# Performance work log

Hardware: AMD Instinct MI355X
Metric: run time of the kernel (lower is better)

The kernel has to match this reference:

```python
import jax, jax.numpy as jnp
import numpy as np

N = 32768   # nodes
E = 131072  # directed edges
B = 8       # graphs in batch
F_IN = 1025
NEG = -1e30
EPS = 1e-5


def _lin_init(k, i, o):
    k1, k2 = jax.random.split(k)
    s = 1.0 / np.sqrt(i)
    return (jax.random.uniform(k1, (i, o), jnp.float32, -s, s),
            jax.random.uniform(k2, (o,), jnp.float32, -s, s))


def _bn_init(k, c):
    k1, k2, k3, k4 = jax.random.split(k, 4)
    gamma = jax.random.uniform(k1, (c,), jnp.float32, 0.5, 1.5)
    beta = jax.random.normal(k2, (c,), jnp.float32) * 0.1
    mean = jax.random.normal(k3, (c,), jnp.float32) * 0.1
    var = jax.random.uniform(k4, (c,), jnp.float32, 0.5, 1.5)
    return jnp.stack([gamma, beta, mean, var])  # [4, c]


def setup_inputs() -> dict:
    key = jax.random.key(0)
    ks = jax.random.split(key, 16)
    x = jax.random.normal(ks[0], (N, F_IN), jnp.float32)
    edge_index = jax.random.randint(ks[1], (2, E), 0, N, dtype=jnp.int32)
    batch = jnp.sort(jax.random.randint(ks[2], (N,), 0, B, dtype=jnp.int32))
    pool_w, pool_b = _lin_init(ks[3], 2 * F_IN, 1)
    c1_w0, _ = _lin_init(ks[4], F_IN, 512)
    c1_w1, c1_b = _lin_init(ks[5], F_IN, 512)
    c2_w0, _ = _lin_init(ks[6], 512, 512)
    c2_w1, c2_b = _lin_init(ks[7], 512, 512)
    bn1 = _bn_init(ks[8], 512)
    bn2 = _bn_init(ks[9], 512)
    bn3 = _bn_init(ks[10], 512)
    bn4 = _bn_init(ks[11], 256)
    lin1_w, lin1_b = _lin_init(ks[12], 1024, 512)
    lin2_w, lin2_b = _lin_init(ks[13], 512, 256)
    lin3_w, lin3_b = _lin_init(ks[14], 256, 4)
    return dict(x=x, edge_index=edge_index, batch=batch,
                pool_w=pool_w, pool_b=pool_b,
                c1_w0=c1_w0, c1_w1=c1_w1, c1_b=c1_b,
                c2_w0=c2_w0, c2_w1=c2_w1, c2_b=c2_b,
                bn1=bn1, bn2=bn2, bn3=bn3, bn4=bn4,
                lin1_w=lin1_w, lin1_b=lin1_b,
                lin2_w=lin2_w, lin2_b=lin2_b,
                lin3_w=lin3_w, lin3_b=lin3_b)


def _batchnorm(h, p):
    g, b, m, v = p[0], p[1], p[2], p[3]
    return (h - m) * jax.lax.rsqrt(v + EPS) * g + b


def _cheb(h, row, col, w, w0, w1, b):
    # ChebConv K=2, sym norm, lambda_max=2: out = h@W0 + (L_hat h)@W1 + b,
    # L_hat = -D^{-1/2} A D^{-1/2} (self-loops removed, diag of scaled L is 0)
    deg = jax.ops.segment_sum(w, row, num_segments=N)
    dis = jnp.where(deg > 0, 1.0 / jnp.sqrt(jnp.maximum(deg, 1e-12)), 0.0)
    nrm = -w * dis[row] * dis[col]
    tx1 = jax.ops.segment_sum(nrm[:, None] * h[row], col, num_segments=N)
    return h @ w0 + tx1 @ w1 + b


def _forward(x, edge_index, batch, pool_w, pool_b,
             c1_w0, c1_w1, c1_b, c2_w0, c2_w1, c2_b,
             bn1, bn2, bn3, bn4,
             lin1_w, lin1_b, lin2_w, lin2_b, lin3_w, lin3_b):
    u, v = edge_index[0], edge_index[1]

    # ---- EdgePooling: edge scores = softmax over dst segments, +0.5 ----
    e = (jnp.concatenate([x[u], x[v]], axis=1) @ pool_w + pool_b)[:, 0]  # [E]
    m = jax.ops.segment_max(e, v, num_segments=N)
    ex = jnp.exp(e - m[v])
    score = ex / jax.ops.segment_sum(ex, v, num_segments=N)[v] + 0.5

    # ---- greedy maximal matching in descending score order ----
    order = jnp.argsort(-score)

    def step(used, k):
        uu, vv = u[k], v[k]
        ok = jnp.logical_not(used[uu] | used[vv])
        used = used.at[uu].set(used[uu] | ok)
        used = used.at[vv].set(used[vv] | ok)
        return used, ok

    _, ok_sorted = jax.lax.scan(step, jnp.zeros((N,), bool), order)
    sel = jnp.zeros((E,), bool).at[order].set(ok_sorted)

    rep = jnp.minimum(u, v)  # cluster representative of a merged edge
    cluster = jnp.arange(N, dtype=jnp.int32)
    cluster = cluster.at[jnp.where(sel, u, N)].set(rep, mode='drop')
    cluster = cluster.at[jnp.where(sel, v, N)].set(rep, mode='drop')
    node_score = jnp.ones((N,), x.dtype).at[jnp.where(sel, rep, N)].set(score, mode='drop')
    px = jnp.zeros_like(x).at[cluster].add(x) * node_score[:, None]  # pooled node feats
    valid = cluster == jnp.arange(N, dtype=jnp.int32)  # surviving cluster rows

    # ---- coarsened edge_index, coalesced (dedup), self-loops dropped ----
    cu, cv = cluster[u], cluster[v]
    nonloop = cu != cv
    key = jnp.where(nonloop, cu * N + cv, N * N + jnp.arange(E, dtype=jnp.int32))
    o2 = jnp.argsort(key)
    sk = key[o2]
    first = jnp.concatenate([jnp.ones((1,), bool), sk[1:] != sk[:-1]])
    keep_sorted = first & (sk < N * N)
    w = jnp.zeros((E,), x.dtype).at[o2].set(keep_sorted.astype(x.dtype))

    # ---- two ChebConv + BN(eval) + ReLU ----
    h = jax.nn.relu(_batchnorm(_cheb(px, cu, cv, w, c1_w0, c1_w1, c1_b), bn1))
    h = jax.nn.relu(_batchnorm(_cheb(h, cu, cv, w, c2_w0, c2_w1, c2_b), bn2))

    # ---- global max + mean pool over valid nodes per graph ----
    hmax = jax.ops.segment_max(jnp.where(valid[:, None], h, NEG), batch, num_segments=B)
    cnt = jax.ops.segment_sum(valid.astype(h.dtype), batch, num_segments=B)
    hmean = jax.ops.segment_sum(jnp.where(valid[:, None], h, 0.0), batch,
                                num_segments=B) / jnp.maximum(cnt, 1.0)[:, None]
    g = jnp.concatenate([hmax, hmean], axis=1)  # [B, 1024]

    # ---- readout MLP (dropout off in eval) ----
    g = jax.nn.relu(_batchnorm(g @ lin1_w + lin1_b, bn3))
    g = jax.nn.relu(_batchnorm(g @ lin2_w + lin2_b, bn4))
    feature = g
    out = jax.nn.log_softmax(jax.nn.relu(g @ lin3_w + lin3_b), axis=-1)
    return out, feature


def reference(x, edge_index, batch, pool_w, pool_b,
              c1_w0, c1_w1, c1_b, c2_w0, c2_w1, c2_b,
              bn1, bn2, bn3, bn4,
              lin1_w, lin1_b, lin2_w, lin2_b, lin3_w, lin3_b):
    return _forward(x, edge_index, batch, pool_w, pool_b,
                    c1_w0, c1_w1, c1_b, c2_w0, c2_w1, c2_b,
                    bn1, bn2, bn3, bn4,
                    lin1_w, lin1_b, lin2_w, lin2_b, lin3_w, lin3_b)
```

## Files before the change

kernel.cpp:

```cpp
#include <hip/hip_runtime.h>
#include <hip/hip_bf16.h>
#include <cstdint>
#include <cmath>

typedef unsigned int u32;
typedef unsigned long long u64;
typedef float f32x4 __attribute__((ext_vector_type(4)));
typedef __bf16 bf16x8 __attribute__((ext_vector_type(8)));
typedef unsigned short us8 __attribute__((ext_vector_type(8)));
typedef unsigned short us4 __attribute__((ext_vector_type(4)));

#define NN 32768
#define NE 131072
#define FIN 1025
#define HTS 262144
#define HTM (HTS - 1)

#define WS_A_D    0ul
#define WS_B_D    262144ul
#define WS_EMAX   524288ul
#define WS_SSUM   655360ul
#define WS_EXD    917504ul
#define WS_CIN    917504ul
#define WS_KEY    1966080ul
#define WS_BEST   3014656ul
#define WS_USED   3276800ul
#define WS_CUR    3276800ul
#define WS_ACT0   3407872ul
#define WS_ACT1   3932160ul
#define WS_BTHI   0ul
#define WS_BT2    3407872ul
#define WS_HT     1966080ul
#define WS_RACC1  2097152ul
#define WS_RACC2  2113536ul
#define WS_CIDX   2129920ul
#define WS_PERM   2260992ul
#define WS_SCORE  4456448ul
#define WS_CSRA   4456448ul
#define WS_SEL    4980736ul
#define WS_CSRC   4980736ul
#define WS_CLUST  5505024ul
#define WS_OTHER  5636096ul
#define WS_NSC    5767168ul
#define WS_CEU    5898240ul
#define WS_CEV    6422528ul
#define WS_DEG    6946816ul
#define WS_OFF    6946816ul
#define WS_DIS    7077888ul
#define WS_PXL    7077888ul
#define WS_MISC   7208960ul
#define WS_GMAX   7209216ul
#define WS_GSUM   7225600ul
#define WS_GCNT   7241984ul
#define WS_P      7242240ul
#define WS_PB     74351104ul
#define WS_H      141459968ul

__device__ __forceinline__ u32 enc_f(float f) {
    u32 b = __float_as_uint(f);
    return (b & 0x80000000u) ? ~b : (b | 0x80000000u);
}
__device__ __forceinline__ float dec_f(u32 m) {
    return (m & 0x80000000u) ? __uint_as_float(m ^ 0x80000000u) : __uint_as_float(~m);
}
__device__ __forceinline__ double wave_sum(double v) {
    #pragma unroll
    for (int off = 32; off > 0; off >>= 1) v += __shfl_down(v, off, 64);
    return v;
}
__device__ __forceinline__ unsigned short f2bf(float v) {
    u32 b = __float_as_uint(v);
    u32 r = b + 0x7FFFu + ((b >> 16) & 1u);
    return (unsigned short)(r >> 16);
}
__device__ __forceinline__ float bf2f(unsigned short h) {
    return __uint_as_float(((u32)h) << 16);
}
__device__ __forceinline__ bf16x8 ld_frag(const unsigned short* p) {
    union { us8 u; bf16x8 b; } t;
    t.u = *(const us8*)p;
    return t.b;
}
__device__ __forceinline__ void dma16(unsigned short* lds, const unsigned short* g) {
    __builtin_amdgcn_global_load_lds((const __attribute__((address_space(1))) u32*)g,
                                     (__attribute__((address_space(3))) u32*)lds, 16, 0, 0);
}

__global__ void node_dots(const float* __restrict__ x, const float* __restrict__ pw,
                          double* a_d, double* b_d,
                          u32* emax, double* ssum, u32* deg, int* misc,
                          u32* gmaxb, float* gsum, float* gcnt,
                          u64* best, u32* used, int* clus, int* other, float* nsc) {
    int gid = blockIdx.x * blockDim.x + threadIdx.x;
    if (gid < NN) {
        emax[gid] = 0u; ssum[gid] = 0.0; deg[gid] = 0u;
        best[gid] = ~0ull; used[gid] = 0u;
        clus[gid] = gid; other[gid] = -1; nsc[gid] = 1.0f;
    }
    if (gid < 4096) { gmaxb[gid] = 0u; gsum[gid] = 0.0f; }
    if (gid < 64) { misc[gid] = (gid == 1) ? NE : 0; gcnt[gid] = 0.0f; }

    int wave = gid >> 6;
    int lane = threadIdx.x & 63;
    if (wave >= NN) return;
    const float* xr = x + (size_t)wave * FIN;
    double s0 = 0.0, s1 = 0.0;
    for (int f = lane; f < FIN; f += 64) {
        double xv = (double)xr[f];
        s0 += xv * (double)pw[f];
        s1 += xv * (double)pw[FIN + f];
    }
    s0 = wave_sum(s0); s1 = wave_sum(s1);
    if (lane == 0) { a_d[wave] = s0; b_d[wave] = s1; }
}

__global__ void edge_p1(const int* __restrict__ ei, const double* __restrict__ a_d,
                        const double* __restrict__ b_d, const float* __restrict__ pb,
                        double* e_d, u32* emax) {
    int k = blockIdx.x * 256 + threadIdx.x;
    if (k >= NE) return;
    int u = ei[k], v = ei[NE + k];
    double e = a_d[u] + b_d[v] + (double)pb[0];
    e_d[k] = e;
    atomicMax(&emax[v], enc_f((float)e));
}
__global__ void edge_p2(const int* __restrict__ ei, double* e_d,
                        const u32* __restrict__ emax, double* ssum) {
    int k = blockIdx.x * 256 + threadIdx.x;
    if (k >= NE) return;
    int v = ei[NE + k];
    float mf = dec_f(emax[v]);
    double ex = exp(e_d[k] - (double)mf);
    e_d[k] = ex;
    unsafeAtomicAdd(&ssum[v], ex);
}
__global__ void edge_p3(const int* __restrict__ ei, const double* __restrict__ e_d,
                        const double* __restrict__ ssum, float* score, u64* key,
                        int* sel, int* act0, u64* best) {
    int k = blockIdx.x * 256 + threadIdx.x;
    if (k >= NE) return;
    int u = ei[k], v = ei[NE + k];
    float sc = (float)(e_d[k] / ssum[v] + 0.5);
    score[k] = sc;
    u32 m = enc_f(sc);
    u64 kk = ((u64)(m ^ 0xFFFFFFFFu) << 32) | (u32)k;
    key[k] = kk;
    sel[k] = 0;
    act0[k] = k;
    atomicMin(&best[u], kk);
    atomicMin(&best[v], kk);
}

__global__ void mk_sel(const u64* __restrict__ key, const int* __restrict__ ei,
                       const int* __restrict__ act, const int* __restrict__ cntp,
                       int* ncntp, const u64* __restrict__ best,
                       u32* used, int* sel) {
    int cnt = cntp[0];
    int stride = gridDim.x * blockDim.x;
    int gid = blockIdx.x * blockDim.x + threadIdx.x;
    if (gid == 0) ncntp[0] = 0;
    for (int i = gid; i < cnt; i += stride) {
        int e = act[i];
        u64 k = key[e];
        int a = ei[e], b = ei[NE + e];
        if (best[a] == k && best[b] == k) { sel[e] = 1; used[a] = 1u; used[b] = 1u; }
    }
}
__global__ void mk_compact(const int* __restrict__ ei, const int* __restrict__ act,
                           const int* __restrict__ cntp, int* nxt, int* ncntp,
                           u64* best, const u32* __restrict__ used) {
    int cnt = cntp[0];
    int stride = gridDim.x * blockDim.x;
    for (int i = blockIdx.x * blockDim.x + threadIdx.x; i < cnt; i += stride) {
        int e = act[i];
        int a = ei[e], b = ei[NE + e];
        best[a] = ~0ull; best[b] = ~0ull;
        bool live = !(used[a] | used[b]);
        u64 mask = __ballot(live);
        if (mask) {
            int lane = threadIdx.x & 63;
            int leader = __ffsll((unsigned long long)mask) - 1;
            int base = 0;
            if (lane == leader) base = atomicAdd(ncntp, __popcll(mask));
            base = __shfl(base, leader, 64);
            if (live) nxt[base + __popcll(mask & ((1ull << lane) - 1ull))] = e;
        }
    }
}
__global__ void mk_min(const u64* __restrict__ key, const int* __restrict__ ei,
                       const int* __restrict__ act, const int* __restrict__ cntp,
                       u64* best) {
    int cnt = cntp[0];
    int stride = gridDim.x * blockDim.x;
    for (int i = blockIdx.x * blockDim.x + threadIdx.x; i < cnt; i += stride) {
        int e = act[i];
        u64 k = key[e];
        atomicMin(&best[ei[e]], k);
        atomicMin(&best[ei[NE + e]], k);
    }
}
__global__ void __launch_bounds__(1024) match_fin(
        const u64* __restrict__ key, const int* __restrict__ ei,
        int* sel, u64* best, u32* used,
        int* listA, int* listB, const int* __restrict__ cntp) {
    int tid = threadIdx.x;
    int cnt = cntp[0];
    int* cur = listA; int* nxt = listB;
    __shared__ int s_n;
    for (int round = 0; round < 4096 && cnt > 0; ++round) {
        for (int i = tid; i < cnt; i += 1024) {
            int e = cur[i]; u64 k = key[e];
            atomicMin(&best[ei[e]], k);
            atomicMin(&best[ei[NE + e]], k);
        }
        __syncthreads();
        for (int i = tid; i < cnt; i += 1024) {
            int e = cur[i]; u64 k = key[e];
            int a = ei[e], b = ei[NE + e];
            if (best[a] == k && best[b] == k) { sel[e] = 1; used[a] = 1u; used[b] = 1u; }
        }
        if (tid == 0) s_n = 0;
        __syncthreads();
        for (int i = tid; i < cnt; i += 1024) {
            int e = cur[i];
            int a = ei[e], b = ei[NE + e];
            best[a] = ~0ull; best[b] = ~0ull;
            if (!(used[a] | used[b])) {
                int idx = atomicAdd(&s_n, 1);
                nxt[idx] = e;
            }
        }
        __syncthreads();
        cnt = s_n;
        int* t = cur; cur = nxt; nxt = t;
        __syncthreads();
    }
}

__global__ void apply_sel(const int* __restrict__ ei, const int* __restrict__ sel,
                          const float* __restrict__ score,
                          int* cluster, int* other, float* nscore,
                          u32* ht, u32* cin) {
    int e = blockIdx.x * 256 + threadIdx.x;
    ht[e << 1] = 0xFFFFFFFFu;
    ht[(e << 1) + 1] = 0xFFFFFFFFu;
    if (e < NN) cin[e] = 0u;
    if (sel[e] != 1) return;
    int u = ei[e], v = ei[NE + e];
    int rep = min(u, v);
    cluster[u] = rep; cluster[v] = rep;
    if (u != v) other[rep] = u + v - rep;
    nscore[rep] = score[e];
}

__global__ void coarse_build(const int* __restrict__ ei, const int* __restrict__ cluster,
                             u32* ht, int* misc, int* ce_u, int* ce_v, u32* deg,
                             u32* cin) {
    int e = blockIdx.x * 256 + threadIdx.x;
    if (e >= NE) return;
    int cu = cluster[ei[e]], cv = cluster[ei[NE + e]];
    if (cu == cv) return;
    u32 k = (u32)cu * 32768u + (u32)cv;
    u32 h = ((k * 2654435761u) >> 12) & HTM;
    while (true) {
        u32 old = atomicCAS(&ht[h], 0xFFFFFFFFu, k);
        if (old == 0xFFFFFFFFu) {
            int idx = atomicAdd(&misc[0], 1);
            ce_u[idx] = cu; ce_v[idx] = cv;
            atomicAdd(&deg[cu], 1u);
            atomicAdd(&cin[cv], 1u);
            break;
        }
        if (old == k) break;
        h = (h + 1) & HTM;
    }
}
__global__ void dis_kernel(const u32* __restrict__ deg, float* dis,
                           float* racc1, float* racc2,
                           const int* __restrict__ clus, const int* __restrict__ batch,
                           float* gcnt) {
    int n = blockIdx.x * 256 + threadIdx.x;
    if (n >= NN) return;
    u32 d = deg[n];
    dis[n] = d ? (float)(1.0 / sqrt((double)d)) : 0.0f;
    if (n < 4096) racc1[n] = 0.0f;
    if (n < 2048) racc2[n] = 0.0f;
    bool val = (clus[n] == n);
    int bt = batch[n];
    int lane = threadIdx.x & 63;
    #pragma unroll
    for (int g = 0; g < 8; ++g) {
        u64 m = __ballot(val && bt == g);
        if (m && lane == (__ffsll((unsigned long long)m) - 1))
            unsafeAtomicAdd(&gcnt[g], (float)__popcll(m));
    }
}

__global__ void __launch_bounds__(1024) scan_kernel(const u32* __restrict__ cin,
                                                    int* off, int* cur,
                                                    const int* __restrict__ clus,
                                                    int* cidx, int* perm, int* misc) {
    __shared__ int part[1024];
    int t = threadIdx.x;
    int base = t << 5;
    int loc[32];
    int s = 0;
    #pragma unroll
    for (int i = 0; i < 32; ++i) { loc[i] = s; s += (int)cin[base + i]; }
    part[t] = s;
    __syncthreads();
    for (int d = 1; d < 1024; d <<= 1) {
        int v = (t >= d) ? part[t - d] : 0;
        __syncthreads();
        if (t >= d) part[t] += v;
        __syncthreads();
    }
    int pre = (t == 0) ? 0 : part[t - 1];
    #pragma unroll
    for (int i = 0; i < 32; ++i) {
        int v = pre + loc[i];
        off[base + i] = v;
        cur[base + i] = v;
    }
    __syncthreads();
    u32 vmask = 0;
    s = 0;
    #pragma unroll
    for (int i = 0; i < 32; ++i) {
        int f = (clus[base + i] == base + i) ? 1 : 0;
        loc[i] = s; s += f;
        vmask |= (u32)f << i;
    }
    part[t] = s;
    __syncthreads();
    for (int d = 1; d < 1024; d <<= 1) {
        int v = (t >= d) ? part[t - d] : 0;
        __syncthreads();
        if (t >= d) part[t] += v;
        __syncthreads();
    }
    int pre2 = (t == 0) ? 0 : part[t - 1];
    #pragma unroll
    for (int i = 0; i < 32; ++i) {
        int c = pre2 + loc[i];
        cidx[base + i] = c;
        if ((vmask >> i) & 1u) perm[c] = base + i;
    }
    if (t == 1023) misc[4] = pre2 + s;
}
__global__ void csr_scatter(const int* __restrict__ ce_u, const int* __restrict__ ce_v,
                            const float* __restrict__ dis, const int* __restrict__ misc,
                            int* cur, int* csr_a, float* csr_c,
                            const int* __restrict__ cidx) {
    int e = blockIdx.x * 256 + threadIdx.x;
    if (e >= misc[0]) return;
    int a = ce_u[e], b = ce_v[e];
    int pos = atomicAdd(&cur[b], 1);
    csr_a[pos] = cidx[a];
    csr_c[pos] = -dis[a] * dis[b];
}

__device__ __forceinline__ size_t pk_idx(int r, int k, int KT) {
    return ((((size_t)(r >> 4) * KT + (k >> 5)) << 6) + (((k >> 3) & 3) << 4) + (r & 15)) << 3;
}

__global__ void __launch_bounds__(256) conv_all(
        const float* __restrict__ x, const int* __restrict__ perm,
        const int* __restrict__ misc,
        const int* __restrict__ other, const float* __restrict__ nsc,
        unsigned short* __restrict__ Abf, float* __restrict__ pxl,
        const float* __restrict__ B10, const float* __restrict__ B11,
        unsigned short* __restrict__ Bp1,
        const float* __restrict__ B20, const float* __restrict__ B21,
        unsigned short* __restrict__ Bp2) {
    int bid = blockIdx.x;
    int t = threadIdx.x;
    if (bid < 2048) {
        int cnt = misc[4];
        int tile = bid;
        if ((tile << 4) >= ((cnt + 127) & ~127)) return;
        int wave = t >> 6, lane = t & 63;
        int l16 = lane & 15, quad = lane >> 4;
        int ci = (tile << 4) + l16;
        bool valid = ci < cnt;
        int row = valid ? perm[ci] : 0;
        int o = valid ? other[row] : -1;
        float s = valid ? nsc[row] : 0.0f;
        const float* xr = x + (size_t)row * FIN;
        const float* xo = x + (size_t)(o >= 0 ? o : row) * FIN;
        for (int kt = wave; kt < 32; kt += 4) {
            int c0 = (kt << 5) + (quad << 3);
            unsigned short h[8];
            #pragma unroll
            for (int j = 0; j < 8; ++j) {
                float v = 0.0f;
                if (valid) {
                    v = xr[c0 + j];
                    if (o >= 0) v += xo[c0 + j];
                    v *= s;
                }
                h[j] = f2bf(v);
            }
            *(us8*)&Abf[((((size_t)tile << 5) + kt) << 9) + ((size_t)lane << 3)] = *(const us8*)h;
        }
        if (t < 16) {
            int ci2 = (tile << 4) + t;
            float v = 0.0f;
            if (ci2 < cnt) {
                int r2 = perm[ci2];
                int o2 = other[r2];
                v = x[(size_t)r2 * FIN + 1024];
                if (o2 >= 0) v += x[(size_t)o2 * FIN + 1024];
                v *= nsc[r2];
            }
            pxl[ci2] = v;
        }
    } else if (bid < 2560) {
        int j = bid - 2048;
        int n = ((j & 3) << 8) + t;
        int k0 = (j >> 2) << 3;
        unsigned short h[8];
        #pragma unroll
        for (int jj = 0; jj < 8; ++jj) {
            int k = k0 + jj;
            float v = (n < 512) ? B10[(size_t)k * 512 + n] : B11[(size_t)k * 512 + (n - 512)];
            h[jj] = f2bf(v);
        }
        *(us8*)&Bp1[pk_idx(n, k0, 32)] = *(const us8*)h;
    } else {
        int j = bid - 2560;
        int n = ((j & 3) << 8) + t;
        int k0 = (j >> 2) << 3;
        unsigned short h[8];
        #pragma unroll
        for (int jj = 0; jj < 8; ++jj) {
            int k = k0 + jj;
            float v = (n < 512) ? B20[(size_t)k * 512 + n] : B21[(size_t)k * 512 + (n - 512)];
            h[jj] = f2bf(v);
        }
        *(us8*)&Bp2[pk_idx(n, k0, 16)] = *(const us8*)h;
    }
}

template <bool R1>
__global__ void __launch_bounds__(256, 4) gemm_pk(
        const unsigned short* __restrict__ Ap, const unsigned short* __restrict__ Bp,
        float* __restrict__ P, unsigned short* __restrict__ Pb, int KT,
        const float* __restrict__ pxl, const float* __restrict__ w0,
        const float* __restrict__ w1, const int* __restrict__ msc) {
    __shared__ unsigned short L[2][8192];
    int tid = threadIdx.x;
    int bid = blockIdx.x;
    int loc = bid >> 3;
    int bn = (loc & 7) << 7;
    int bm = ((((bid & 7) << 5) | (loc >> 3))) << 7;
    if (bm >= ((msc[4] + 127) & ~127)) return;
    int wave = tid >> 6, lane = tid & 63, quad = lane >> 4, l16 = lane & 15;
    int moff = (wave >> 1) << 6, noff = (wave & 1) << 6;
    f32x4 acc[4][4];
    #pragma unroll
    for (int i = 0; i < 4; ++i)
        #pragma unroll
        for (int j = 0; j < 4; ++j) acc[i][j] = (f32x4){0.f, 0.f, 0.f, 0.f};

    const unsigned short* src[4];
    unsigned short* dst[4];
    #pragma unroll
    for (int q = 0; q < 4; ++q) {
        int f = (wave << 2) + q;
        int tg = (f < 8) ? ((bm >> 4) + f) : ((bn >> 4) + (f - 8));
        src[q] = ((f < 8) ? Ap : Bp) + (((size_t)tg * KT) << 9) + ((size_t)lane << 3);
        dst[q] = &L[0][(size_t)f << 9];
    }
    const unsigned short* ra = &L[0][(size_t)(wave >> 1) << 11];
    const unsigned short* rb = &L[0][4096 + ((size_t)(wave & 1) << 11)];

    #pragma unroll
    for (int q = 0; q < 4; ++q) dma16(dst[q], src[q]);
    __syncthreads();

    int cur = 0;
    for (int kt = 0; kt < KT; ++kt) {
        if (kt + 1 < KT) {
            int nb = (cur ^ 1) * 8192;
            size_t go = ((size_t)(kt + 1)) << 9;
            #pragma unroll
            for (int q = 0; q < 4; ++q) dma16(dst[q] + nb, src[q] + go);
        }
        const unsigned short* la = ra + cur * 8192;
        const unsigned short* lb = rb + cur * 8192;
        bf16x8 af[4], bf[4];
        #pragma unroll
        for (int i = 0; i < 4; ++i) {
            af[i] = ld_frag(la + ((size_t)i << 9) + (lane << 3));
            bf[i] = ld_frag(lb + ((size_t)i << 9) + (lane << 3));
        }
        #pragma unroll
        for (int mi = 0; mi < 4; ++mi)
            #pragma unroll
            for (int ni = 0; ni < 4; ++ni)
                acc[mi][ni] = __builtin_amdgcn_mfma_f32_16x16x32_bf16(af[mi], bf[ni], acc[mi][ni], 0, 0, 0);
        __syncthreads();
        cur ^= 1;
    }
    #pragma unroll
    for (int mi = 0; mi < 4; ++mi)
        #pragma unroll
        for (int ni = 0; ni < 4; ++ni) {
            int col = bn + noff + (ni << 4) + l16;
            float wl = 0.0f;
            if (R1) wl = (col < 512) ? w0[524288 + col] : w1[524288 + col - 512];
            #pragma unroll
            for (int r2 = 0; r2 < 4; ++r2) {
                int row = bm + moff + (mi << 4) + (quad << 2) + r2;
                float v = acc[mi][ni][r2];
                if (R1) v += pxl[row] * wl;
                if (col < 512) P[(size_t)row * 512 + col] = v;
                else Pb[(size_t)row * 512 + (col - 512)] = f2bf(v);
            }
        }
}

template <bool BF16OUT>
__global__ void __launch_bounds__(256) cheb_fuse(
        const float* __restrict__ P, const unsigned short* __restrict__ Pb,
        const int* __restrict__ off,
        const int* __restrict__ csr_a, const float* __restrict__ csr_c,
        const int* __restrict__ misc, const float* __restrict__ bias,
        const float* __restrict__ bn, float* __restrict__ Hf,
        unsigned short* __restrict__ Hb, const int* __restrict__ perm) {
    int b = (blockIdx.x * 256 + threadIdx.x) >> 6;
    int lane = threadIdx.x & 63;
    if (b >= misc[4]) return;
    int r = perm[b];
    int s = off[r];
    int e = (r < NN - 1) ? off[r + 1] : misc[0];
    int c0 = lane << 3;
    float a0[4], a1[4];
    {
        float4 t0 = *(const float4*)&P[(size_t)b * 512 + c0];
        float4 t1 = *(const float4*)&P[(size_t)b * 512 + c0 + 4];
        a0[0] = t0.x; a0[1] = t0.y; a0[2] = t0.z; a0[3] = t0.w;
        a1[0] = t1.x; a1[1] = t1.y; a1[2] = t1.z; a1[3] = t1.w;
    }
    for (int j = s; j < e; ++j) {
        int a = csr_a[j];
        float cf = csr_c[j];
        us8 raw = *(const us8*)&Pb[(size_t)a * 512 + c0];
        a0[0] = fmaf(cf, bf2f(raw[0]), a0[0]); a0[1] = fmaf(cf, bf2f(raw[1]), a0[1]);
        a0[2] = fmaf(cf, bf2f(raw[2]), a0[2]); a0[3] = fmaf(cf, bf2f(raw[3]), a0[3]);
        a1[0] = fmaf(cf, bf2f(raw[4]), a1[0]); a1[1] = fmaf(cf, bf2f(raw[5]), a1[1]);
        a1[2] = fmaf(cf, bf2f(raw[6]), a1[2]); a1[3] = fmaf(cf, bf2f(raw[7]), a1[3]);
    }
    float o[8];
    #pragma unroll
    for (int i = 0; i < 8; ++i) {
        int j = c0 + i;
        float acc = (i < 4) ? a0[i] : a1[i - 4];
        float ga = bn[j], be = bn[512 + j], mn = bn[1024 + j], vr = bn[1536 + j];
        float sc = (float)(1.0 / sqrt((double)vr + 1e-5));
        float v = (acc + bias[j] - mn) * sc * ga + be;
        o[i] = v > 0.0f ? v : 0.0f;
    }
    if (BF16OUT) {
        unsigned short h[8];
        #pragma unroll
        for (int i = 0; i < 8; ++i) h[i] = f2bf(o[i]);
        *(us8*)&Hb[pk_idx(b, c0, 16)] = *(const us8*)h;
    } else {
        *(float4*)&Hf[(size_t)b * 512 + c0] = make_float4(o[0], o[1], o[2], o[3]);
        *(float4*)&Hf[(size_t)b * 512 + c0 + 4] = make_float4(o[4], o[5], o[6], o[7]);
    }
}

__global__ void __launch_bounds__(256) pool_kernel(
        const float* __restrict__ H, const int* __restrict__ cluster,
        const int* __restrict__ batch, u32* gmaxb, float* gsum,
        const int* __restrict__ cidx) {
    int t = threadIdx.x;
    int n0 = blockIdx.x * 64;
    float m0 = 0.0f, m1 = 0.0f, s0 = 0.0f, s1 = 0.0f;
    int cur = batch[n0];
    for (int i = 0; i < 64; ++i) {
        int n = n0 + i;
        int bt = batch[n];
        if (bt != cur) {
            atomicMax(&gmaxb[cur * 512 + t], __float_as_uint(m0));
            atomicMax(&gmaxb[cur * 512 + t + 256], __float_as_uint(m1));
            unsafeAtomicAdd(&gsum[cur * 512 + t], s0);
            unsafeAtomicAdd(&gsum[cur * 512 + t + 256], s1);
            m0 = m1 = s0 = s1 = 0.0f; cur = bt;
        }
        if (cluster[n] == n) {
            size_t ci = (size_t)cidx[n];
            float h0 = H[ci * 512 + t];
            float h1 = H[ci * 512 + t + 256];
            m0 = fmaxf(m0, h0); m1 = fmaxf(m1, h1);
            s0 += h0; s1 += h1;
        }
    }
    atomicMax(&gmaxb[cur * 512 + t], __float_as_uint(m0));
    atomicMax(&gmaxb[cur * 512 + t + 256], __float_as_uint(m1));
    unsafeAtomicAdd(&gsum[cur * 512 + t], s0);
    unsafeAtomicAdd(&gsum[cur * 512 + t + 256], s1);
}

__global__ void __launch_bounds__(512) ro1(
        const u32* __restrict__ gmaxb, const float* __restrict__ gsum,
        const float* __restrict__ gcnt, const float* __restrict__ l1w,
        float* __restrict__ racc1) {
    int o = threadIdx.x;
    int k0 = blockIdx.x << 4;
    float acc[8] = {0, 0, 0, 0, 0, 0, 0, 0};
    float inv[8];
    #pragma unroll
    for (int b = 0; b < 8; ++b) inv[b] = 1.0f / fmaxf(gcnt[b], 1.0f);
    for (int kk = 0; kk < 16; ++kk) {
        int k = k0 + kk;
        float w = l1w[(size_t)k * 512 + o];
        #pragma unroll
        for (int b = 0; b < 8; ++b) {
            float g = (k < 512) ? __uint_as_float(gmaxb[b * 512 + k])
                                : gsum[b * 512 + (k - 512)] * inv[b];
            acc[b] = fmaf(g, w, acc[b]);
        }
    }
    #pragma unroll
    for (int b = 0; b < 8; ++b) unsafeAtomicAdd(&racc1[b * 512 + o], acc[b]);
}
__global__ void __launch_bounds__(256) ro3(
        const float* __restrict__ racc1, const float* __restrict__ l1b,
        const float* __restrict__ bn3, const float* __restrict__ l2w,
        float* __restrict__ racc2) {
    int o = threadIdx.x;
    int k0 = blockIdx.x << 4;
    float acc[8] = {0, 0, 0, 0, 0, 0, 0, 0};
    for (int kk = 0; kk < 16; ++kk) {
        int k = k0 + kk;
        float ga = bn3[k], be = bn3[512 + k], mn = bn3[1024 + k], vr = bn3[1536 + k];
        float sc = (float)(1.0 / sqrt((double)vr + 1e-5));
        float bi = l1b[k];
        float w = l2w[(size_t)k * 256 + o];
        #pragma unroll
        for (int b = 0; b < 8; ++b) {
            float g1 = (racc1[b * 512 + k] + bi - mn) * sc * ga + be;
            g1 = g1 > 0.0f ? g1 : 0.0f;
            acc[b] = fmaf(g1, w, acc[b]);
        }
    }
    #pragma unroll
    for (int b = 0; b < 8; ++b) unsafeAtomicAdd(&racc2[b * 256 + o], acc[b]);
}
__global__ void __launch_bounds__(256) ro4(
        const float* __restrict__ racc2, const float* __restrict__ l2b,
        const float* __restrict__ bn4, const float* __restrict__ l3w,
        const float* __restrict__ l3b, float* __restrict__ out) {
    __shared__ float G2[8 * 256];
    int o = threadIdx.x;
    {
        float ga = bn4[o], be = bn4[256 + o], mn = bn4[512 + o], vr = bn4[768 + o];
        float sc = (float)(1.0 / sqrt((double)vr + 1e-5));
        float bi = l2b[o];
        #pragma unroll
        for (int b = 0; b < 8; ++b) {
            float v = (racc2[b * 256 + o] + bi - mn) * sc * ga + be;
            v = v > 0.0f ? v : 0.0f;
            G2[b * 256 + o] = v;
            out[32 + b * 256 + o] = v;
        }
    }
    __syncthreads();
    if (o < 8) {
        int b = o;
        float r[4];
        #pragma unroll
        for (int c = 0; c < 4; ++c) {
            float acc = l3b[c];
            for (int k = 0; k < 256; ++k) acc += G2[b * 256 + k] * l3w[k * 4 + c];
            r[c] = acc > 0.0f ? acc : 0.0f;
        }
        float mx = fmaxf(fmaxf(r[0], r[1]), fmaxf(r[2], r[3]));
        float s = 0.0f;
        #pragma unroll
        for (int c = 0; c < 4; ++c) s += expf(r[c] - mx);
        float lse = mx + logf(s);
        #pragma unroll
        for (int c = 0; c < 4; ++c) out[b * 4 + c] = r[c] - lse;
    }
}

extern "C" void kernel_launch(void* const* d_in, const int* in_sizes, int n_in,
                              void* d_out, int out_size, void* d_ws, size_t ws_size,
                              hipStream_t stream) {
    const float* x      = (const float*)d_in[0];
    const int*   ei     = (const int*)d_in[1];
    const int*   batch  = (const int*)d_in[2];
    const float* pool_w = (const float*)d_in[3];
    const float* pool_b = (const float*)d_in[4];
    const float* c1_w0  = (const float*)d_in[5];
    const float* c1_w1  = (const float*)d_in[6];
    const float* c1_b   = (const float*)d_in[7];
    const float* c2_w0  = (const float*)d_in[8];
    const float* c2_w1  = (const float*)d_in[9];
    const float* c2_b   = (const float*)d_in[10];
    const float* bn1    = (const float*)d_in[11];
    const float* bn2    = (const float*)d_in[12];
    const float* bn3    = (const float*)d_in[13];
    const float* bn4    = (const float*)d_in[14];
    const float* l1w    = (const float*)d_in[15];
    const float* l1b    = (const float*)d_in[16];
    const float* l2w    = (const float*)d_in[17];
    const float* l2b    = (const float*)d_in[18];
    const float* l3w    = (const float*)d_in[19];
    const float* l3b    = (const float*)d_in[20];
    float* out = (float*)d_out;
    char* ws = (char*)d_ws;

    double* a_d   = (double*)(ws + WS_A_D);
    double* b_d   = (double*)(ws + WS_B_D);
    u32*    emax  = (u32*)(ws + WS_EMAX);
    double* ssum  = (double*)(ws + WS_SSUM);
    double* exd   = (double*)(ws + WS_EXD);
    u32*    cin   = (u32*)(ws + WS_CIN);
    int*    cidxp = (int*)(ws + WS_CIDX);
    int*    permp = (int*)(ws + WS_PERM);
    u64*    key   = (u64*)(ws + WS_KEY);
    u64*    best  = (u64*)(ws + WS_BEST);
    u32*    used  = (u32*)(ws + WS_USED);
    int*    curp  = (int*)(ws + WS_CUR);
    int*    act0  = (int*)(ws + WS_ACT0);
    int*    act1  = (int*)(ws + WS_ACT1);
    unsigned short* bthi = (unsigned short*)(ws + WS_BTHI);
    unsigned short* bt2  = (unsigned short*)(ws + WS_BT2);
    float*  pxl   = (float*)(ws + WS_PXL);
    u32*    ht    = (u32*)(ws + WS_HT);
    float*  racc1 = (float*)(ws + WS_RACC1);
    float*  racc2 = (float*)(ws + WS_RACC2);
    float*  score = (float*)(ws + WS_SCORE);
    int*    csr_a = (int*)(ws + WS_CSRA);
    int*    sel   = (int*)(ws + WS_SEL);
    float*  csr_c = (float*)(ws + WS_CSRC);
    int*    clus  = (int*)(ws + WS_CLUST);
    int*    other = (int*)(ws + WS_OTHER);
    float*  nsc   = (float*)(ws + WS_NSC);
    int*    ce_u  = (int*)(ws + WS_CEU);
    int*    ce_v  = (int*)(ws + WS_CEV);
    u32*    deg   = (u32*)(ws + WS_DEG);
    int*    off   = (int*)(ws + WS_OFF);
    float*  dis   = (float*)(ws + WS_DIS);
    int*    misc  = (int*)(ws + WS_MISC);
    u32*    gmaxb = (u32*)(ws + WS_GMAX);
    float*  gsum  = (float*)(ws + WS_GSUM);
    float*  gcnt  = (float*)(ws + WS_GCNT);
    float*  P     = (float*)(ws + WS_P);
    unsigned short* Pb = (unsigned short*)(ws + WS_PB);
    unsigned short* ax = (unsigned short*)(ws + WS_H);
    unsigned short* hb = (unsigned short*)(ws + WS_H);
    float*  H     = (float*)(ws + WS_H);

    node_dots<<<NN / 4, 256, 0, stream>>>(x, pool_w, a_d, b_d,
                                          emax, ssum, deg, misc, gmaxb, gsum, gcnt,
                                          best, used, clus, other, nsc);
    edge_p1<<<NE / 256, 256, 0, stream>>>(ei, a_d, b_d, pool_b, exd, emax);
    edge_p2<<<NE / 256, 256, 0, stream>>>(ei, exd, emax, ssum);
    edge_p3<<<NE / 256, 256, 0, stream>>>(ei, exd, ssum, score, key, sel, act0, best);

    {
        static const int gr[9] = {512, 512, 256, 128, 64, 32, 16, 8, 8};
        int* acts[2] = {act0, act1};
        for (int r = 0; r < 8; ++r) {
            int c = r & 1, n = 1 - c;
            mk_sel<<<gr[r], 256, 0, stream>>>(key, ei, acts[c], &misc[1 + c],
                                              &misc[1 + n], best, used, sel);
            mk_compact<<<gr[r], 256, 0, stream>>>(ei, acts[c], &misc[1 + c],
                                                  acts[n], &misc[1 + n], best, used);
            mk_min<<<gr[r + 1], 256, 0, stream>>>(key, ei, acts[n], &misc[1 + n], best);
        }
        match_fin<<<1, 1024, 0, stream>>>(key, ei, sel, best, used,
                                          act0, act1, &misc[1]);
    }

    apply_sel<<<NE / 256, 256, 0, stream>>>(ei, sel, score, clus, other, nsc, ht, cin);
    coarse_build<<<NE / 256, 256, 0, stream>>>(ei, clus, ht, misc, ce_u, ce_v, deg, cin);
    dis_kernel<<<NN / 256, 256, 0, stream>>>(deg, dis, racc1, racc2, clus, batch, gcnt);
    scan_kernel<<<1, 1024, 0, stream>>>(cin, off, curp, clus, cidxp, permp, misc);
    csr_scatter<<<NE / 256, 256, 0, stream>>>(ce_u, ce_v, dis, misc, curp, csr_a, csr_c,
                                              cidxp);

    conv_all<<<2816, 256, 0, stream>>>(x, permp, misc, other, nsc, ax, pxl,
                                       c1_w0, c1_w1, bthi, c2_w0, c2_w1, bt2);
    gemm_pk<true><<<2048, 256, 0, stream>>>(ax, bthi, P, Pb, 32, pxl, c1_w0, c1_w1, misc);
    cheb_fuse<true><<<NN / 4, 256, 0, stream>>>(P, Pb, off, csr_a, csr_c, misc, c1_b, bn1,
                                                nullptr, hb, permp);

    gemm_pk<false><<<2048, 256, 0, stream>>>(hb, bt2, P, Pb, 16, nullptr, nullptr, nullptr,
                                             misc);
    cheb_fuse<false><<<NN / 4, 256, 0, stream>>>(P, Pb, off, csr_a, csr_c, misc, c2_b, bn2,
                                                 H, nullptr, permp);

    pool_kernel<<<NN / 64, 256, 0, stream>>>(H, clus, batch, gmaxb, gsum, cidxp);

    ro1<<<64, 512, 0, stream>>>(gmaxb, gsum, gcnt, l1w, racc1);
    ro3<<<32, 256, 0, stream>>>(racc1, l1b, bn3, l2w, racc2);
    ro4<<<1, 256, 0, stream>>>(racc2, l2b, bn4, l3w, l3b, out);
}
```

Measured before the change: 839.5 us.

## Replace single-block prefix scan with three-phase multi-block scan

Splits the single 1024-thread scan kernel into a per-block reduction, a small scan over block sums, and a per-block finishing scan across 128 blocks. The final pass packs the two prefix counts into one integer so both come out of a single shared-memory scan. The aim is to remove the serial bottleneck of one workgroup walking all 32768 entries. The cost is two extra kernel launches and a second read of the inputs.

```diff
diff --git a/kernel.cpp b/kernel.cpp
--- a/kernel.cpp
+++ b/kernel.cpp
@@ -35,6 +35,8 @@
 #define WS_RACC2  2113536ul
 #define WS_CIDX   2129920ul
 #define WS_PERM   2260992ul
+#define WS_BSUM   2392064ul
+#define WS_BOFF   2393088ul
 #define WS_SCORE  4456448ul
 #define WS_CSRA   4456448ul
 #define WS_SEL    4980736ul
@@ -296,58 +298,70 @@
     }
 }
 
-__global__ void __launch_bounds__(1024) scan_kernel(const u32* __restrict__ cin,
-                                                    int* off, int* cur,
-                                                    const int* __restrict__ clus,
-                                                    int* cidx, int* perm, int* misc) {
-    __shared__ int part[1024];
+__global__ void __launch_bounds__(256) scan_part(const u32* __restrict__ cin,
+                                                 const int* __restrict__ clus,
+                                                 int* __restrict__ bsum) {
     int t = threadIdx.x;
-    int base = t << 5;
-    int loc[32];
-    int s = 0;
-    #pragma unroll
-    for (int i = 0; i < 32; ++i) { loc[i] = s; s += (int)cin[base + i]; }
-    part[t] = s;
+    int i = blockIdx.x * 256 + t;
+    int vc = (int)cin[i];
+    int vv = (clus[i] == i) ? 1 : 0;
+    #pragma unroll
+    for (int off = 32; off > 0; off >>= 1) {
+        vc += __shfl_down(vc, off, 64);
+        vv += __shfl_down(vv, off, 64);
+    }
+    __shared__ int sc[4], sv[4];
+    if ((t & 63) == 0) { sc[t >> 6] = vc; sv[t >> 6] = vv; }
     __syncthreads();
-    for (int d = 1; d < 1024; d <<= 1) {
-        int v = (t >= d) ? part[t - d] : 0;
+    if (t == 0) {
+        bsum[blockIdx.x] = sc[0] + sc[1] + sc[2] + sc[3];
+        bsum[128 + blockIdx.x] = sv[0] + sv[1] + sv[2] + sv[3];
+    }
+}
+__global__ void __launch_bounds__(128) scan_mid(const int* __restrict__ bsum,
+                                                int* __restrict__ boff, int* misc) {
+    __shared__ int s[256];
+    int t = threadIdx.x;
+    int v0 = bsum[t], v1 = bsum[128 + t];
+    s[t] = v0; s[128 + t] = v1;
+    __syncthreads();
+    for (int d = 1; d < 128; d <<= 1) {
+        int a = (t >= d) ? s[t - d] : 0;
+        int b = (t >= d) ? s[128 + t - d] : 0;
         __syncthreads();
-        if (t >= d) part[t] += v;
+        if (t >= d) { s[t] += a; s[128 + t] += b; }
         __syncthreads();
     }
-    int pre = (t == 0) ? 0 : part[t - 1];
-    #pragma unroll
-    for (int i = 0; i < 32; ++i) {
-        int v = pre + loc[i];
-        off[base + i] = v;
-        cur[base + i] = v;
-    }
+    boff[t] = s[t] - v0;
+    boff[128 + t] = s[128 + t] - v1;
+    if (t == 127) misc[4] = s[255];
+}
+__global__ void __launch_bounds__(256) scan_fin(const u32* __restrict__ cin,
+                                                const int* __restrict__ clus,
+                                                const int* __restrict__ boff,
+                                                int* off, int* cur, int* cidx, int* perm) {
+    __shared__ int s[256];
+    int t = threadIdx.x;
+    int i = blockIdx.x * 256 + t;
+    int vc = (int)cin[i];
+    int vv = (clus[i] == i) ? 1 : 0;
+    int p = (vc << 9) | vv;
+    s[t] = p;
     __syncthreads();
-    u32 vmask = 0;
-    s = 0;
-    #pragma unroll
-    for (int i = 0; i < 32; ++i) {
-        int f = (clus[base + i] == base + i) ? 1 : 0;
-        loc[i] = s; s += f;
-        vmask |= (u32)f << i;
-    }
-    part[t] = s;
-    __syncthreads();
-    for (int d = 1; d < 1024; d <<= 1) {
-        int v = (t >= d) ? part[t - d] : 0;
+    for (int d = 1; d < 256; d <<= 1) {
+        int a = (t >= d) ? s[t - d] : 0;
         __syncthreads();
-        if (t >= d) part[t] += v;
+        if (t >= d) s[t] += a;
         __syncthreads();
     }
-    int pre2 = (t == 0) ? 0 : part[t - 1];
-    #pragma unroll
-    for (int i = 0; i < 32; ++i) {
-        int c = pre2 + loc[i];
-        cidx[base + i] = c;
-        if ((vmask >> i) & 1u) perm[c] = base + i;
-    }
-    if (t == 1023) misc[4] = pre2 + s;
-}
+    int ex = s[t] - p;
+    int o = boff[blockIdx.x] + (ex >> 9);
+    off[i] = o; cur[i] = o;
+    int c = boff[128 + blockIdx.x] + (ex & 511);
+    cidx[i] = c;
+    if (vv) perm[c] = i;
+}
+
 __global__ void csr_scatter(const int* __restrict__ ce_u, const int* __restrict__ ce_v,
                             const float* __restrict__ dis, const int* __restrict__ misc,
                             int* cur, int* csr_a, float* csr_c,
@@ -724,6 +738,8 @@
     u32*    cin   = (u32*)(ws + WS_CIN);
     int*    cidxp = (int*)(ws + WS_CIDX);
     int*    permp = (int*)(ws + WS_PERM);
+    int*    bsum  = (int*)(ws + WS_BSUM);
+    int*    boffp = (int*)(ws + WS_BOFF);
     u64*    key   = (u64*)(ws + WS_KEY);
     u64*    best  = (u64*)(ws + WS_BEST);
     u32*    used  = (u32*)(ws + WS_USED);
@@ -783,7 +799,9 @@
     apply_sel<<<NE / 256, 256, 0, stream>>>(ei, sel, score, clus, other, nsc, ht, cin);
     coarse_build<<<NE / 256, 256, 0, stream>>>(ei, clus, ht, misc, ce_u, ce_v, deg, cin);
     dis_kernel<<<NN / 256, 256, 0, stream>>>(deg, dis, racc1, racc2, clus, batch, gcnt);
-    scan_kernel<<<1, 1024, 0, stream>>>(cin, off, curp, clus, cidxp, permp, misc);
+    scan_part<<<128, 256, 0, stream>>>(cin, clus, bsum);
+    scan_mid<<<1, 128, 0, stream>>>(bsum, boffp, misc);
+    scan_fin<<<128, 256, 0, stream>>>(cin, clus, boffp, off, curp, cidxp, permp);
     csr_scatter<<<NE / 256, 256, 0, stream>>>(ce_u, ce_v, dis, misc, curp, csr_a, csr_c,
                                               cidxp);
 
```

After: 761.9 us. 1.1x faster.
